# Performance work log

Measured on AMD Instinct MI355X. Metric: run time of the kernel, lower is better.

The kernel has to match this reference:

```python
import jax, jax.numpy as jnp
import numpy as np

D_MODEL = 1024
EPS = 1e-6

def setup_inputs() -> dict:
    key = jax.random.key(0)
    ks = jax.random.split(key, 13)
    B, T, S, E = 4, 2048, 2048, D_MODEL
    s = 1.0 / np.sqrt(E)
    return {
        "query": jax.random.normal(ks[0], (B, T, E), jnp.float32),
        "key": jax.random.normal(ks[1], (B, S, E), jnp.float32),
        "value": jax.random.normal(ks[2], (B, S, E), jnp.float32),
        "Wq": jax.random.normal(ks[3], (E, E), jnp.float32) * s,
        "bq": jax.random.normal(ks[4], (E,), jnp.float32) * 0.01,
        "Wk": jax.random.normal(ks[5], (E, E), jnp.float32) * s,
        "bk": jax.random.normal(ks[6], (E,), jnp.float32) * 0.01,
        "Wv": jax.random.normal(ks[7], (E, E), jnp.float32) * s,
        "bv": jax.random.normal(ks[8], (E,), jnp.float32) * 0.01,
        "Wo": jax.random.normal(ks[9], (E, E), jnp.float32) * s,
        "bo": jax.random.normal(ks[10], (E,), jnp.float32) * 0.01,
        "gamma": jnp.ones((E,), jnp.float32),
        "beta": jnp.zeros((E,), jnp.float32),
    }

def reference(query, key, value, Wq, bq, Wk, bk, Wv, bv, Wo, bo, gamma, beta):
    # Note: despite the name, the original never splits heads; attention is
    # over the full d_model with scale 1/sqrt(d_model). Dropout = eval identity.
    residual = query
    q = jnp.einsum('bte,fe->btf', query, Wq) + bq   # nn.Linear: x @ W.T + b
    k = jnp.einsum('bse,fe->bsf', key, Wk) + bk
    v = jnp.einsum('bse,fe->bsf', value, Wv) + bv
    scores = jnp.einsum('bte,bse->bts', q, k) / jnp.sqrt(jnp.float32(D_MODEL))
    attn = jax.nn.softmax(scores, axis=-1)          # (B, T, S)
    ctx = jnp.einsum('bts,bse->bte', attn, v)
    out = jnp.einsum('bte,fe->btf', ctx, Wo) + bo
    out = out + residual
    mu = jnp.mean(out, axis=-1, keepdims=True)
    var = jnp.mean(jnp.square(out - mu), axis=-1, keepdims=True)
    return (out - mu) * jax.lax.rsqrt(var + EPS) * gamma + beta
```

## Files before the change

kernel.cpp:

```cpp
#include <hip/hip_runtime.h>
#include <hip/hip_bf16.h>

typedef __bf16 bf16_t;
typedef __bf16 bf16x4 __attribute__((ext_vector_type(4)));
typedef __bf16 bf16x8 __attribute__((ext_vector_type(8)));
typedef float f32x4 __attribute__((ext_vector_type(4)));

#define E_DIM 1024
#define SEQ   2048
#define NBATCH 4

#define BARR()  asm volatile("s_barrier" ::: "memory")
#define LGKM0() asm volatile("s_waitcnt lgkmcnt(0)" ::: "memory")
#define VMC6()  asm volatile("s_waitcnt vmcnt(6)" ::: "memory")
#define VMC0()  asm volatile("s_waitcnt vmcnt(0)" ::: "memory")

__global__ __launch_bounds__(256) void k_cast_all(
    const float* __restrict__ q, const float* __restrict__ k, const float* __restrict__ v,
    const float* __restrict__ wq, const float* __restrict__ wk,
    const float* __restrict__ wv, const float* __restrict__ wo,
    bf16_t* __restrict__ xq, bf16_t* __restrict__ xk, bf16_t* __restrict__ xv,
    bf16_t* __restrict__ wqb, bf16_t* __restrict__ wkb,
    bf16_t* __restrict__ wvb, bf16_t* __restrict__ wob) {
  const int b = blockIdx.x;
  const float* s; bf16_t* d; long base;
  if (b < 4096)        { s = q; d = xq; base = (long)b * 2048; }
  else if (b < 8192)   { s = k; d = xk; base = (long)(b - 4096) * 2048; }
  else if (b < 12288)  { s = v; d = xv; base = (long)(b - 8192) * 2048; }
  else {
    const int w = (b - 12288) >> 9, r = (b - 12288) & 511;
    s = (w == 0) ? wq : (w == 1) ? wk : (w == 2) ? wv : wo;
    d = (w == 0) ? wqb : (w == 1) ? wkb : (w == 2) ? wvb : wob;
    base = (long)r * 2048;
  }
  const long i = base + threadIdx.x * 8;
  const float4 a = *(const float4*)(s + i);
  const float4 c = *(const float4*)(s + i + 4);
  bf16x8 o;
  o[0] = (bf16_t)a.x; o[1] = (bf16_t)a.y; o[2] = (bf16_t)a.z; o[3] = (bf16_t)a.w;
  o[4] = (bf16_t)c.x; o[5] = (bf16_t)c.y; o[6] = (bf16_t)c.z; o[7] = (bf16_t)c.w;
  *(bf16x8*)(d + i) = o;
}

template <int OUTMODE, bool RS, bool QKV3, int REPS, int NTL>
__global__ __launch_bounds__(256, 2) void k_g13(
    const bf16_t* __restrict__ A, int lda, long sA,
    const bf16_t* __restrict__ B, int ldb, long sB,
    void* __restrict__ Cv, int ldc, long sC,
    float scale, const float* __restrict__ bias,
    const float* __restrict__ residual, int GM, int GN,
    const bf16_t* __restrict__ A1, const bf16_t* __restrict__ A2,
    const bf16_t* __restrict__ B1, const bf16_t* __restrict__ B2,
    const float* __restrict__ bias1, const float* __restrict__ bias2,
    void* __restrict__ Cv1, void* __restrict__ Cv2) {
  constexpr int ASZ   = 16384;
  constexpr int BUFSZ = 32768;
  constexpr int NT    = 1 << NTL;
  constexpr int TT    = REPS << NTL;
  extern __shared__ char smem[];

  const int tid  = threadIdx.x;
  const int lane = tid & 63;
  const int wid  = tid >> 6;
  const int wm   = wid >> 1;
  const int wn   = wid & 1;
  const int l15  = lane & 15;
  const int lq   = lane >> 4;

  const int nwg  = gridDim.x;
  const int orig = blockIdx.x;
  const int wg   = (orig & 7) * (nwg >> 3) + (orig >> 3);

  const int colk = ((tid & 7) ^ ((tid >> 3) & 7)) << 3;
  const int trow = tid >> 3;
  const int ldsw = wid << 10;

  const bf16_t *pA0, *pB0, *pA1 = nullptr, *pB1 = nullptr, *pA2 = nullptr, *pB2 = nullptr;
  int zzr0 = 0, bmr0 = 0, bnr0 = 0, zzr1 = 0, bmr1 = 0, bnr1 = 0;
  if constexpr (QKV3) {
    bmr0 = wg / GN; bnr0 = wg - bmr0 * GN;
    const long aoff = (long)(bmr0 * 128 + trow) * lda + colk;
    const long boff = (long)(bnr0 * 128 + trow) * ldb + colk;
    pA0 = A + aoff;  pA1 = A1 + aoff;  pA2 = A2 + aoff;
    pB0 = B + boff;  pB1 = B1 + boff;  pB2 = B2 + boff;
  } else {
    {
      const int g  = wg;
      zzr0 = g / (GM * GN);
      const int rm = g - zzr0 * (GM * GN);
      bmr0 = rm / GN; bnr0 = rm - bmr0 * GN;
      pA0 = A + zzr0 * sA + (long)(bmr0 * 128 + trow) * lda + colk;
      pB0 = B + zzr0 * sB + (long)(bnr0 * 128 + trow) * ldb + colk;
    }
    if constexpr (REPS >= 2) {
      const int g  = nwg + wg;
      zzr1 = g / (GM * GN);
      const int rm = g - zzr1 * (GM * GN);
      bmr1 = rm / GN; bnr1 = rm - bmr1 * GN;
      pA1 = A + zzr1 * sA + (long)(bmr1 * 128 + trow) * lda + colk;
      pB1 = B + zzr1 * sB + (long)(bnr1 * 128 + trow) * ldb + colk;
    }
  }

#define GLL(gaddr, ldsoff)                                                       \
  __builtin_amdgcn_global_load_lds(                                             \
      (const __attribute__((address_space(1))) void*)(gaddr),                   \
      (__attribute__((address_space(3))) void*)(smem + (ldsoff)), 16, 0, 0)

  auto stA = [&](int tau, int buf) {
    tau = tau < TT ? tau : TT - 1;
    const int rep = tau >> NTL;
    const bf16_t* p = (REPS == 1) ? pA0
                    : (REPS == 2) ? (rep ? pA1 : pA0)
                    : (rep == 0 ? pA0 : (rep == 1 ? pA1 : pA2));
    p += (long)(tau & (NT - 1)) * 64;
#pragma unroll
    for (int s = 0; s < 4; ++s)
      GLL(p + (long)(s * 32) * lda, buf * BUFSZ + s * 4096 + ldsw);
  };
  auto stB = [&](int tau, int buf, int half) {
    tau = tau < TT ? tau : TT - 1;
    const int rep = tau >> NTL;
    const bf16_t* p = (REPS == 1) ? pB0
                    : (REPS == 2) ? (rep ? pB1 : pB0)
                    : (rep == 0 ? pB0 : (rep == 1 ? pB1 : pB2));
    p += (long)(tau & (NT - 1)) * 64;
#pragma unroll
    for (int s = 0; s < 2; ++s)
      GLL(p + (long)(half * 64 + s * 32) * ldb,
          buf * BUFSZ + ASZ + half * 8192 + s * 4096 + ldsw);
  };

  f32x4 acc[4][4];
#pragma unroll
  for (int m = 0; m < 4; ++m)
#pragma unroll
    for (int n = 0; n < 4; ++n) acc[m][n] = (f32x4){0.f, 0.f, 0.f, 0.f};
  f32x4 rs[4];
#pragma unroll
  for (int m = 0; m < 4; ++m) rs[m] = (f32x4){0.f, 0.f, 0.f, 0.f};
  bf16x8 vones;
#pragma unroll
  for (int i = 0; i < 8; ++i) vones[i] = (bf16_t)1.0f;

  auto ldA = [&](bf16x8 (&a)[2][2], int cur, int mq) {
#pragma unroll
    for (int i = 0; i < 2; ++i) {
      const int row = wm * 64 + (mq * 2 + i) * 16 + l15;
#pragma unroll
      for (int kk = 0; kk < 2; ++kk) {
        const int byt = cur * BUFSZ + row * 128 + ((kk * 64 + lq * 16) ^ ((row & 7) << 4));
        a[i][kk] = *(const bf16x8*)(smem + byt);
      }
    }
  };
  auto ldB = [&](bf16x8 (&b)[2][2], int cur, int nq) {
#pragma unroll
    for (int n2 = 0; n2 < 2; ++n2) {
      const int row = wn * 64 + (nq * 2 + n2) * 16 + l15;
#pragma unroll
      for (int kk = 0; kk < 2; ++kk) {
        const int byt = cur * BUFSZ + ASZ + row * 128 + ((kk * 64 + lq * 16) ^ ((row & 7) << 4));
        b[n2][kk] = *(const bf16x8*)(smem + byt);
      }
    }
  };
  auto mmaq = [&](bf16x8 (&a)[2][2], bf16x8 (&b)[2][2], int mq, int nq) {
    __builtin_amdgcn_s_setprio(1);
#pragma unroll
    for (int kk = 0; kk < 2; ++kk)
#pragma unroll
      for (int i = 0; i < 2; ++i)
#pragma unroll
        for (int n2 = 0; n2 < 2; ++n2)
          acc[mq * 2 + i][nq * 2 + n2] = __builtin_amdgcn_mfma_f32_16x16x32_bf16(
              a[i][kk], b[n2][kk], acc[mq * 2 + i][nq * 2 + n2], 0, 0, 0);
    __builtin_amdgcn_s_setprio(0);
  };
  auto mmars = [&](bf16x8 (&a)[2][2], int mq) {
#pragma unroll
    for (int kk = 0; kk < 2; ++kk)
#pragma unroll
      for (int i = 0; i < 2; ++i)
        rs[mq * 2 + i] = __builtin_amdgcn_mfma_f32_16x16x32_bf16(
            a[i][kk], vones, rs[mq * 2 + i], 0, 0, 0);
  };

  stB(0, 0, 0); stB(0, 0, 1); stA(0, 0);
  stB(1, 1, 0); stA(1, 1);
  VMC6();
  BARR();

  bf16x8 a0[2][2], a1[2][2], b0[2][2], b1[2][2];
  auto tile = [&](int t, int cur) {
    ldA(a0, cur, 0); ldB(b0, cur, 0);
    stB(t + 1, cur ^ 1, 1);
    BARR(); LGKM0();
    mmaq(a0, b0, 0, 0);
    BARR();
    ldB(b1, cur, 1);
    BARR(); LGKM0();
    mmaq(a0, b1, 0, 1);
    if constexpr (RS) mmars(a0, 0);
    BARR();
    ldA(a1, cur, 1);
    stB(t + 2, cur, 0);
    BARR(); LGKM0();
    mmaq(a1, b1, 1, 1);
    BARR();
    stA(t + 2, cur);
    BARR();
    mmaq(a1, b0, 1, 0);
    if constexpr (RS) mmars(a1, 1);
    VMC6();
    BARR();
  };

#pragma unroll
  for (int rep = 0; rep < REPS; ++rep) {
    const int tb = rep << NTL;
    for (int tt = 0; tt < NT; tt += 2) {
      tile(tb + tt, 0);
      tile(tb + tt + 1, 1);
    }

    {
      int zz2, bm2, bn2;
      const float* biasp;
      void* Cvp;
      bool tr = false;
      if constexpr (QKV3) {
        zz2 = 0; bm2 = bmr0; bn2 = bnr0;
        biasp = rep == 0 ? bias : (rep == 1 ? bias1 : bias2);
        Cvp   = rep == 0 ? Cv   : (rep == 1 ? Cv1   : Cv2);
        tr = (rep == 2);
      } else {
        zz2 = (REPS >= 2 && rep) ? zzr1 : zzr0;
        bm2 = (REPS >= 2 && rep) ? bmr1 : bmr0;
        bn2 = (REPS >= 2 && rep) ? bnr1 : bnr0;
        biasp = bias; Cvp = Cv;
      }
      const int colb = bn2 * 128 + wn * 64 + l15;
      const int rowb = bm2 * 128 + wm * 64 + lq * 4;
#pragma unroll
      for (int m = 0; m < 4; ++m) {
        float inv[4];
        if constexpr (RS) {
#pragma unroll
          for (int j = 0; j < 4; ++j) inv[j] = 1.0f / rs[m][j];
        }
#pragma unroll
        for (int n = 0; n < 4; ++n) {
          const int colg = colb + n * 16;
          float bval = 0.0f;
          if constexpr (OUTMODE != 3) bval = biasp ? biasp[colg] : 0.0f;
          if (QKV3 && tr) {
            const int r0 = rowb + m * 16;
            bf16x4 pk;
#pragma unroll
            for (int j = 0; j < 4; ++j) pk[j] = (bf16_t)(acc[m][n][j] * scale + bval);
            const long bb = (long)(r0 >> 11);
            const int ss = r0 & (SEQ - 1);
            *(bf16x4*)((bf16_t*)Cvp + bb * ((long)E_DIM * SEQ) + (long)colg * SEQ + ss) = pk;
          } else {
#pragma unroll
            for (int j = 0; j < 4; ++j) {
              const int r = rowb + m * 16 + j;
              float v;
              if constexpr (OUTMODE == 3) v = __expf(acc[m][n][j] * scale);
              else v = acc[m][n][j] * scale + bval;
              if constexpr (RS) v *= inv[j];
              if (OUTMODE == 0 && residual) v += residual[(long)r * ldc + colg];
              const long idx = (long)zz2 * sC + (long)r * ldc + colg;
              if constexpr (OUTMODE == 0) ((float*)Cvp)[idx] = v;
              else ((bf16_t*)Cvp)[idx] = (bf16_t)v;
            }
          }
        }
      }
      if (rep + 1 < REPS) {
#pragma unroll
        for (int m = 0; m < 4; ++m) {
#pragma unroll
          for (int n = 0; n < 4; ++n) acc[m][n] = (f32x4){0.f, 0.f, 0.f, 0.f};
          rs[m] = (f32x4){0.f, 0.f, 0.f, 0.f};
        }
      }
    }
  }
  VMC0();
#undef GLL
}

__global__ __launch_bounds__(256) void k_layernorm(float* __restrict__ out,
                                                   const float* __restrict__ gamma,
                                                   const float* __restrict__ beta) {
  const long row = blockIdx.x;
  float* rp = out + row * 1024;
  const int t = threadIdx.x;
  const float4 v = *(const float4*)(rp + t * 4);
  float s = v.x + v.y + v.z + v.w;
#pragma unroll
  for (int o = 32; o; o >>= 1) s += __shfl_xor(s, o);
  __shared__ float red1[4], red2[4];
  const int lane = t & 63, w = t >> 6;
  if (lane == 0) red1[w] = s;
  __syncthreads();
  const float mu = (red1[0] + red1[1] + red1[2] + red1[3]) * (1.0f / 1024.0f);
  const float d0 = v.x - mu, d1 = v.y - mu, d2 = v.z - mu, d3 = v.w - mu;
  float ss = d0 * d0 + d1 * d1 + d2 * d2 + d3 * d3;
#pragma unroll
  for (int o = 32; o; o >>= 1) ss += __shfl_xor(ss, o);
  if (lane == 0) red2[w] = ss;
  __syncthreads();
  const float var = (red2[0] + red2[1] + red2[2] + red2[3]) * (1.0f / 1024.0f);
  const float rsq = rsqrtf(var + 1e-6f);
  const float4 g = *(const float4*)(gamma + t * 4);
  const float4 b = *(const float4*)(beta + t * 4);
  float4 o;
  o.x = d0 * rsq * g.x + b.x;
  o.y = d1 * rsq * g.y + b.y;
  o.z = d2 * rsq * g.z + b.z;
  o.w = d3 * rsq * g.w + b.w;
  *(float4*)(rp + t * 4) = o;
}

extern "C" void kernel_launch(void* const* d_in, const int* in_sizes, int n_in,
                              void* d_out, int out_size, void* d_ws, size_t ws_size,
                              hipStream_t stream) {
  const float* query = (const float*)d_in[0];
  const float* key   = (const float*)d_in[1];
  const float* value = (const float*)d_in[2];
  const float* Wq = (const float*)d_in[3];
  const float* bq = (const float*)d_in[4];
  const float* Wk = (const float*)d_in[5];
  const float* bk = (const float*)d_in[6];
  const float* Wv = (const float*)d_in[7];
  const float* bv = (const float*)d_in[8];
  const float* Wo = (const float*)d_in[9];
  const float* bo = (const float*)d_in[10];
  const float* gamma = (const float*)d_in[11];
  const float* beta  = (const float*)d_in[12];
  float* out = (float*)d_out;

  char* ws = (char*)d_ws;
  const size_t XSZ = (size_t)NBATCH * SEQ * E_DIM * 2;
  const size_t WSZ = (size_t)E_DIM * E_DIM * 2;
  const size_t B2  = 3 * XSZ;

  bf16_t* Xq  = (bf16_t*)(ws + 0);
  bf16_t* Xk  = (bf16_t*)(ws + XSZ);
  bf16_t* Xv  = (bf16_t*)(ws + 2 * XSZ);
  bf16_t* SC  = (bf16_t*)(ws + 0);
  bf16_t* Wqb = (bf16_t*)(ws + B2);
  bf16_t* Wkb = (bf16_t*)(ws + B2 + WSZ);
  bf16_t* Wvb = (bf16_t*)(ws + B2 + 2 * WSZ);
  bf16_t* Wob = (bf16_t*)(ws + B2 + 3 * WSZ);
  bf16_t* Qb  = (bf16_t*)(ws + B2 + 4 * WSZ);
  bf16_t* Kb  = (bf16_t*)(ws + B2 + 4 * WSZ + XSZ);
  bf16_t* Vt  = (bf16_t*)(ws + B2 + 4 * WSZ + 2 * XSZ);
  bf16_t* Ctx = (bf16_t*)(ws + B2 + 4 * WSZ + 3 * XSZ);

  const int NTOK = NBATCH * SEQ;
  const int SMB = 65536;

  hipFuncSetAttribute((const void*)k_g13<1, false, true, 3, 4>, hipFuncAttributeMaxDynamicSharedMemorySize, SMB);
  hipFuncSetAttribute((const void*)k_g13<3, false, false, 2, 4>, hipFuncAttributeMaxDynamicSharedMemorySize, SMB);
  hipFuncSetAttribute((const void*)k_g13<1, true, false, 1, 5>, hipFuncAttributeMaxDynamicSharedMemorySize, SMB);
  hipFuncSetAttribute((const void*)k_g13<0, false, false, 1, 4>, hipFuncAttributeMaxDynamicSharedMemorySize, SMB);

  k_cast_all<<<dim3(14336), 256, 0, stream>>>(query, key, value, Wq, Wk, Wv, Wo,
                                              Xq, Xk, Xv, Wqb, Wkb, Wvb, Wob);

  k_g13<1, false, true, 3, 4><<<512, 256, SMB, stream>>>(
      Xq, E_DIM, 0, Wqb, E_DIM, 0, Qb, E_DIM, 0, 1.0f, bq, nullptr, 64, 8,
      Xk, Xv, Wkb, Wvb, bk, bv, Kb, Vt);

  k_g13<3, false, false, 2, 4><<<512, 256, SMB, stream>>>(
      Qb, E_DIM, (long)SEQ * E_DIM, Kb, E_DIM, (long)SEQ * E_DIM,
      SC, SEQ, (long)SEQ * SEQ, 0.03125f, nullptr, nullptr, 16, 16,
      nullptr, nullptr, nullptr, nullptr, nullptr, nullptr, nullptr, nullptr);

  k_g13<1, true, false, 1, 5><<<512, 256, SMB, stream>>>(
      SC, SEQ, (long)SEQ * SEQ, Vt, SEQ, (long)E_DIM * SEQ,
      Ctx, E_DIM, (long)SEQ * E_DIM, 1.0f, nullptr, nullptr, 16, 8,
      nullptr, nullptr, nullptr, nullptr, nullptr, nullptr, nullptr, nullptr);

  k_g13<0, false, false, 1, 4><<<512, 256, SMB, stream>>>(
      Ctx, E_DIM, 0, Wob, E_DIM, 0, out, E_DIM, 0, 1.0f, bo, query, 64, 8,
      nullptr, nullptr, nullptr, nullptr, nullptr, nullptr, nullptr, nullptr);

  k_layernorm<<<dim3(NTOK), 256, 0, stream>>>(out, gamma, beta);
}
```

Measured before the change: 225.2 us.

## Fuse fp32-to-bf16 activation cast into QKV projection GEMM A-operand loads

The separate cast kernel for query/key/value activations is removed. The QKV GEMM now loads fp32 A tiles into registers, converts them to bf16 and writes them swizzled into LDS, with the global loads issued one tile ahead. This removes a full write and re-read of the bf16 activation copies (about 50MB of traffic). In exchange the A path loses the async global_load_lds, and the GEMM gains register pressure and extra VALU/LDS-store work inside the main loop.

After: 224.9 us. No clear change (-0.1%).

```diff
diff --git a/kernel.cpp b/kernel.cpp
--- a/kernel.cpp
+++ b/kernel.cpp
@@ -13,43 +13,35 @@
 #define BARR()  asm volatile("s_barrier" ::: "memory")
 #define LGKM0() asm volatile("s_waitcnt lgkmcnt(0)" ::: "memory")
 #define VMC6()  asm volatile("s_waitcnt vmcnt(6)" ::: "memory")
+#define VMC2()  asm volatile("s_waitcnt vmcnt(2)" ::: "memory")
 #define VMC0()  asm volatile("s_waitcnt vmcnt(0)" ::: "memory")
 
-__global__ __launch_bounds__(256) void k_cast_all(
-    const float* __restrict__ q, const float* __restrict__ k, const float* __restrict__ v,
+__global__ __launch_bounds__(256) void k_castw(
     const float* __restrict__ wq, const float* __restrict__ wk,
     const float* __restrict__ wv, const float* __restrict__ wo,
-    bf16_t* __restrict__ xq, bf16_t* __restrict__ xk, bf16_t* __restrict__ xv,
     bf16_t* __restrict__ wqb, bf16_t* __restrict__ wkb,
     bf16_t* __restrict__ wvb, bf16_t* __restrict__ wob) {
   const int b = blockIdx.x;
-  const float* s; bf16_t* d; long base;
-  if (b < 4096)        { s = q; d = xq; base = (long)b * 2048; }
-  else if (b < 8192)   { s = k; d = xk; base = (long)(b - 4096) * 2048; }
-  else if (b < 12288)  { s = v; d = xv; base = (long)(b - 8192) * 2048; }
-  else {
-    const int w = (b - 12288) >> 9, r = (b - 12288) & 511;
-    s = (w == 0) ? wq : (w == 1) ? wk : (w == 2) ? wv : wo;
-    d = (w == 0) ? wqb : (w == 1) ? wkb : (w == 2) ? wvb : wob;
-    base = (long)r * 2048;
-  }
-  const long i = base + threadIdx.x * 8;
-  const float4 a = *(const float4*)(s + i);
-  const float4 c = *(const float4*)(s + i + 4);
+  const int w = b >> 9, r = b & 511;
+  const float* s = (w == 0) ? wq : (w == 1) ? wk : (w == 2) ? wv : wo;
+  bf16_t* d = (w == 0) ? wqb : (w == 1) ? wkb : (w == 2) ? wvb : wob;
+  const long i = (long)r * 2048 + threadIdx.x * 8;
+  const f32x4 a = *(const f32x4*)(s + i);
+  const f32x4 c = *(const f32x4*)(s + i + 4);
   bf16x8 o;
-  o[0] = (bf16_t)a.x; o[1] = (bf16_t)a.y; o[2] = (bf16_t)a.z; o[3] = (bf16_t)a.w;
-  o[4] = (bf16_t)c.x; o[5] = (bf16_t)c.y; o[6] = (bf16_t)c.z; o[7] = (bf16_t)c.w;
+  o[0] = (bf16_t)a[0]; o[1] = (bf16_t)a[1]; o[2] = (bf16_t)a[2]; o[3] = (bf16_t)a[3];
+  o[4] = (bf16_t)c[0]; o[5] = (bf16_t)c[1]; o[6] = (bf16_t)c[2]; o[7] = (bf16_t)c[3];
   *(bf16x8*)(d + i) = o;
 }
 
-template <int OUTMODE, bool RS, bool QKV3, int REPS, int NTL>
-__global__ __launch_bounds__(256, 2) void k_g13(
-    const bf16_t* __restrict__ A, int lda, long sA,
+template <int OUTMODE, bool RS, bool QKV3, int REPS, int NTL, bool AF32>
+__global__ __launch_bounds__(256, 2) void k_g14(
+    const void* __restrict__ A, int lda, long sA,
     const bf16_t* __restrict__ B, int ldb, long sB,
     void* __restrict__ Cv, int ldc, long sC,
     float scale, const float* __restrict__ bias,
     const float* __restrict__ residual, int GM, int GN,
-    const bf16_t* __restrict__ A1, const bf16_t* __restrict__ A2,
+    const void* __restrict__ A1, const void* __restrict__ A2,
     const bf16_t* __restrict__ B1, const bf16_t* __restrict__ B2,
     const float* __restrict__ bias1, const float* __restrict__ bias2,
     void* __restrict__ Cv1, void* __restrict__ Cv2) {
@@ -75,21 +67,30 @@
   const int trow = tid >> 3;
   const int ldsw = wid << 10;
 
-  const bf16_t *pA0, *pB0, *pA1 = nullptr, *pB1 = nullptr, *pA2 = nullptr, *pB2 = nullptr;
+  const bf16_t *pA0 = nullptr, *pA1 = nullptr, *pA2 = nullptr;
+  const float  *pAf0 = nullptr, *pAf1 = nullptr, *pAf2 = nullptr;
+  const bf16_t *pB0, *pB1 = nullptr, *pB2 = nullptr;
   int zzr0 = 0, bmr0 = 0, bnr0 = 0, zzr1 = 0, bmr1 = 0, bnr1 = 0;
   if constexpr (QKV3) {
     bmr0 = wg / GN; bnr0 = wg - bmr0 * GN;
-    const long aoff = (long)(bmr0 * 128 + trow) * lda + colk;
     const long boff = (long)(bnr0 * 128 + trow) * ldb + colk;
-    pA0 = A + aoff;  pA1 = A1 + aoff;  pA2 = A2 + aoff;
     pB0 = B + boff;  pB1 = B1 + boff;  pB2 = B2 + boff;
+    if constexpr (AF32) {
+      const long aoff = (long)(bmr0 * 128 + trow) * lda + (tid & 7) * 8;
+      pAf0 = (const float*)A + aoff;  pAf1 = (const float*)A1 + aoff;
+      pAf2 = (const float*)A2 + aoff;
+    } else {
+      const long aoff = (long)(bmr0 * 128 + trow) * lda + colk;
+      pA0 = (const bf16_t*)A + aoff;  pA1 = (const bf16_t*)A1 + aoff;
+      pA2 = (const bf16_t*)A2 + aoff;
+    }
   } else {
     {
       const int g  = wg;
       zzr0 = g / (GM * GN);
       const int rm = g - zzr0 * (GM * GN);
       bmr0 = rm / GN; bnr0 = rm - bmr0 * GN;
-      pA0 = A + zzr0 * sA + (long)(bmr0 * 128 + trow) * lda + colk;
+      pA0 = (const bf16_t*)A + zzr0 * sA + (long)(bmr0 * 128 + trow) * lda + colk;
       pB0 = B + zzr0 * sB + (long)(bnr0 * 128 + trow) * ldb + colk;
     }
     if constexpr (REPS >= 2) {
@@ -97,7 +98,7 @@
       zzr1 = g / (GM * GN);
       const int rm = g - zzr1 * (GM * GN);
       bmr1 = rm / GN; bnr1 = rm - bmr1 * GN;
-      pA1 = A + zzr1 * sA + (long)(bmr1 * 128 + trow) * lda + colk;
+      pA1 = (const bf16_t*)A + zzr1 * sA + (long)(bmr1 * 128 + trow) * lda + colk;
       pB1 = B + zzr1 * sB + (long)(bnr1 * 128 + trow) * ldb + colk;
     }
   }
@@ -108,15 +109,17 @@
       (__attribute__((address_space(3))) void*)(smem + (ldsoff)), 16, 0, 0)
 
   auto stA = [&](int tau, int buf) {
-    tau = tau < TT ? tau : TT - 1;
-    const int rep = tau >> NTL;
-    const bf16_t* p = (REPS == 1) ? pA0
-                    : (REPS == 2) ? (rep ? pA1 : pA0)
-                    : (rep == 0 ? pA0 : (rep == 1 ? pA1 : pA2));
-    p += (long)(tau & (NT - 1)) * 64;
-#pragma unroll
-    for (int s = 0; s < 4; ++s)
-      GLL(p + (long)(s * 32) * lda, buf * BUFSZ + s * 4096 + ldsw);
+    if constexpr (!AF32) {
+      tau = tau < TT ? tau : TT - 1;
+      const int rep = tau >> NTL;
+      const bf16_t* p = (REPS == 1) ? pA0
+                      : (REPS == 2) ? (rep ? pA1 : pA0)
+                      : (rep == 0 ? pA0 : (rep == 1 ? pA1 : pA2));
+      p += (long)(tau & (NT - 1)) * 64;
+#pragma unroll
+      for (int s = 0; s < 4; ++s)
+        GLL(p + (long)(s * 32) * lda, buf * BUFSZ + s * 4096 + ldsw);
+    }
   };
   auto stB = [&](int tau, int buf, int half) {
     tau = tau < TT ? tau : TT - 1;
@@ -131,6 +134,43 @@
           buf * BUFSZ + ASZ + half * 8192 + s * 4096 + ldsw);
   };
 
+  f32x4 a32[8];
+  int wbyt[4];
+#pragma unroll
+  for (int s = 0; s < 4; ++s) {
+    const int row = s * 32 + trow;
+    wbyt[s] = row * 128 + (((tid & 7) * 16) ^ ((row & 7) << 4));
+  }
+  auto ldAg = [&](int tau) {
+    if constexpr (AF32) {
+      tau = tau < TT ? tau : TT - 1;
+      const int rep = tau >> NTL;
+      const float* p = (REPS == 1) ? pAf0
+                     : (REPS == 2) ? (rep ? pAf1 : pAf0)
+                     : (rep == 0 ? pAf0 : (rep == 1 ? pAf1 : pAf2));
+      p += (long)(tau & (NT - 1)) * 64;
+#pragma unroll
+      for (int s = 0; s < 4; ++s) {
+        a32[2 * s]     = *(const f32x4*)(p + (long)(s * 32) * lda);
+        a32[2 * s + 1] = *(const f32x4*)(p + (long)(s * 32) * lda + 4);
+      }
+    }
+  };
+  auto wrA = [&](int buf) {
+    if constexpr (AF32) {
+#pragma unroll
+      for (int s = 0; s < 4; ++s) {
+        bf16x8 w;
+#pragma unroll
+        for (int j = 0; j < 4; ++j) {
+          w[j]     = (bf16_t)a32[2 * s][j];
+          w[4 + j] = (bf16_t)a32[2 * s + 1][j];
+        }
+        *(bf16x8*)(smem + buf * BUFSZ + wbyt[s]) = w;
+      }
+    }
+  };
+
   f32x4 acc[4][4];
 #pragma unroll
   for (int m = 0; m < 4; ++m)
@@ -186,42 +226,59 @@
             a[i][kk], vones, rs[mq * 2 + i], 0, 0, 0);
   };
 
-  stB(0, 0, 0); stB(0, 0, 1); stA(0, 0);
-  stB(1, 1, 0); stA(1, 1);
-  VMC6();
-  BARR();
-
-  bf16x8 a0[2][2], a1[2][2], b0[2][2], b1[2][2];
-  auto tile = [&](int t, int cur) {
-    ldA(a0, cur, 0); ldB(b0, cur, 0);
-    stB(t + 1, cur ^ 1, 1);
-    BARR(); LGKM0();
-    mmaq(a0, b0, 0, 0);
+  if constexpr (AF32) {
+    stB(0, 0, 0); stB(0, 0, 1);
+    ldAg(0);
+    VMC0();
+    wrA(0);
+    ldAg(1);
+    stB(1, 1, 0);
+    VMC2();
+    wrA(1);
+    LGKM0();
     BARR();
-    ldB(b1, cur, 1);
-    BARR(); LGKM0();
-    mmaq(a0, b1, 0, 1);
-    if constexpr (RS) mmars(a0, 0);
-    BARR();
-    ldA(a1, cur, 1);
-    stB(t + 2, cur, 0);
-    BARR(); LGKM0();
-    mmaq(a1, b1, 1, 1);
-    BARR();
-    stA(t + 2, cur);
-    BARR();
-    mmaq(a1, b0, 1, 0);
-    if constexpr (RS) mmars(a1, 1);
+  } else {
+    stB(0, 0, 0); stB(0, 0, 1); stA(0, 0);
+    stB(1, 1, 0); stA(1, 1);
     VMC6();
     BARR();
-  };
+  }
+
+  bf16x8 a0[2][2], a1[2][2], b0[2][2], b1[2][2];
+
+#define TILE_STEP(t_, cur_)                                                     \
+  {                                                                             \
+    ldA(a0, (cur_), 0); ldB(b0, (cur_), 0);                                     \
+    stB((t_) + 1, (cur_) ^ 1, 1);                                               \
+    if constexpr (AF32) ldAg((t_) + 2);                                         \
+    BARR(); LGKM0();                                                            \
+    mmaq(a0, b0, 0, 0);                                                         \
+    BARR();                                                                     \
+    ldB(b1, (cur_), 1);                                                         \
+    BARR(); LGKM0();                                                            \
+    mmaq(a0, b1, 0, 1);                                                         \
+    if constexpr (RS) mmars(a0, 0);                                             \
+    BARR();                                                                     \
+    ldA(a1, (cur_), 1);                                                         \
+    stB((t_) + 2, (cur_), 0);                                                   \
+    BARR(); LGKM0();                                                            \
+    mmaq(a1, b1, 1, 1);                                                         \
+    BARR();                                                                     \
+    if constexpr (!AF32) stA((t_) + 2, (cur_));                                 \
+    BARR();                                                                     \
+    mmaq(a1, b0, 1, 0);                                                         \
+    if constexpr (RS) mmars(a1, 1);                                             \
+    if constexpr (AF32) { VMC2(); wrA((cur_)); LGKM0(); }                       \
+    else VMC6();                                                                \
+    BARR();                                                                     \
+  }
 
 #pragma unroll
   for (int rep = 0; rep < REPS; ++rep) {
     const int tb = rep << NTL;
     for (int tt = 0; tt < NT; tt += 2) {
-      tile(tb + tt, 0);
-      tile(tb + tt + 1, 1);
+      TILE_STEP(tb + tt, 0)
+      TILE_STEP(tb + tt + 1, 1)
     }
 
     {
@@ -289,6 +346,7 @@
     }
   }
   VMC0();
+#undef TILE_STEP
 #undef GLL
 }
 
@@ -348,9 +406,6 @@
   const size_t WSZ = (size_t)E_DIM * E_DIM * 2;
   const size_t B2  = 3 * XSZ;
 
-  bf16_t* Xq  = (bf16_t*)(ws + 0);
-  bf16_t* Xk  = (bf16_t*)(ws + XSZ);
-  bf16_t* Xv  = (bf16_t*)(ws + 2 * XSZ);
   bf16_t* SC  = (bf16_t*)(ws + 0);
   bf16_t* Wqb = (bf16_t*)(ws + B2);
   bf16_t* Wkb = (bf16_t*)(ws + B2 + WSZ);
@@ -364,29 +419,28 @@
   const int NTOK = NBATCH * SEQ;
   const int SMB = 65536;
 
-  hipFuncSetAttribute((const void*)k_g13<1, false, true, 3, 4>, hipFuncAttributeMaxDynamicSharedMemorySize, SMB);
-  hipFuncSetAttribute((const void*)k_g13<3, false, false, 2, 4>, hipFuncAttributeMaxDynamicSharedMemorySize, SMB);
-  hipFuncSetAttribute((const void*)k_g13<1, true, false, 1, 5>, hipFuncAttributeMaxDynamicSharedMemorySize, SMB);
-  hipFuncSetAttribute((const void*)k_g13<0, false, false, 1, 4>, hipFuncAttributeMaxDynamicSharedMemorySize, SMB);
-
-  k_cast_all<<<dim3(14336), 256, 0, stream>>>(query, key, value, Wq, Wk, Wv, Wo,
-                                              Xq, Xk, Xv, Wqb, Wkb, Wvb, Wob);
-
-  k_g13<1, false, true, 3, 4><<<512, 256, SMB, stream>>>(
-      Xq, E_DIM, 0, Wqb, E_DIM, 0, Qb, E_DIM, 0, 1.0f, bq, nullptr, 64, 8,
-      Xk, Xv, Wkb, Wvb, bk, bv, Kb, Vt);
-
-  k_g13<3, false, false, 2, 4><<<512, 256, SMB, stream>>>(
+  hipFuncSetAttribute((const void*)k_g14<1, false, true, 3, 4, true>,  hipFuncAttributeMaxDynamicSharedMemorySize, SMB);
+  hipFuncSetAttribute((const void*)k_g14<3, false, false, 2, 4, false>, hipFuncAttributeMaxDynamicSharedMemorySize, SMB);
+  hipFuncSetAttribute((const void*)k_g14<1, true, false, 1, 5, false>,  hipFuncAttributeMaxDynamicSharedMemorySize, SMB);
+  hipFuncSetAttribute((const void*)k_g14<0, false, false, 1, 4, false>, hipFuncAttributeMaxDynamicSharedMemorySize, SMB);
+
+  k_castw<<<dim3(2048), 256, 0, stream>>>(Wq, Wk, Wv, Wo, Wqb, Wkb, Wvb, Wob);
+
+  k_g14<1, false, true, 3, 4, true><<<512, 256, SMB, stream>>>(
+      query, E_DIM, 0, Wqb, E_DIM, 0, Qb, E_DIM, 0, 1.0f, bq, nullptr, 64, 8,
+      key, value, Wkb, Wvb, bk, bv, Kb, Vt);
+
+  k_g14<3, false, false, 2, 4, false><<<512, 256, SMB, stream>>>(
       Qb, E_DIM, (long)SEQ * E_DIM, Kb, E_DIM, (long)SEQ * E_DIM,
       SC, SEQ, (long)SEQ * SEQ, 0.03125f, nullptr, nullptr, 16, 16,
       nullptr, nullptr, nullptr, nullptr, nullptr, nullptr, nullptr, nullptr);
 
-  k_g13<1, true, false, 1, 5><<<512, 256, SMB, stream>>>(
+  k_g14<1, true, false, 1, 5, false><<<512, 256, SMB, stream>>>(
       SC, SEQ, (long)SEQ * SEQ, Vt, SEQ, (long)E_DIM * SEQ,
       Ctx, E_DIM, (long)SEQ * E_DIM, 1.0f, nullptr, nullptr, 16, 8,
       nullptr, nullptr, nullptr, nullptr, nullptr, nullptr, nullptr, nullptr);
 
-  k_g13<0, false, false, 1, 4><<<512, 256, SMB, stream>>>(
+  k_g14<0, false, false, 1, 4, false><<<512, 256, SMB, stream>>>(
       Ctx, E_DIM, 0, Wob, E_DIM, 0, out, E_DIM, 0, 1.0f, bo, query, 64, 8,
       nullptr, nullptr, nullptr, nullptr, nullptr, nullptr, nullptr, nullptr);
 
```
